# Performance work log

Measured on AMD Instinct MI355X. Metric: run time of the kernel, lower is better.

The kernel has to match this reference:

```python
import jax, jax.numpy as jnp
import numpy as np

EPS = 1e-6   # param.eps
DT = 1e-2    # param.dt
DX = 1.0     # param.dx
DY = 1.0     # param.dy
N_PARAM = 1.0  # param.N


def _lap(c, dx=1.0, dy=1.0):
    # 5-point periodic Laplacian stencil on the last two dims
    return ((jnp.roll(c, 1, -1) + jnp.roll(c, -1, -1) - 2.0 * c) / (dx * dx)
            + (jnp.roll(c, 1, -2) + jnp.roll(c, -1, -2) - 2.0 * c) / (dy * dy))


def _log_with_mask(m, eps=EPS):
    # masked positions get constant eps -> zero gradient there, like torch masked_fill
    return jnp.log(jnp.where(m < eps, eps, m))


def setup_inputs() -> dict:
    key = jax.random.key(0)
    ks = jax.random.split(key, 12)
    B, H, W = 8, 1024, 1024
    inp = {
        "cv": jax.random.uniform(ks[0], (B, H, W), dtype=jnp.float32),
        "ci": jax.random.uniform(ks[1], (B, H, W), dtype=jnp.float32),
        "eta": jax.random.uniform(ks[2], (B, H, W), dtype=jnp.float32),
    }
    names = ["energy_v0", "energy_i0", "kBT0", "kappa_v0", "kappa_i0",
             "kappa_eta0", "diff_v0", "diff_i0", "L0"]
    for i, n in enumerate(names):
        inp[n] = jax.random.uniform(ks[3 + i], (1,), dtype=jnp.float32)
    return inp


def reference(cv, ci, eta, energy_v0, energy_i0, kBT0, kappa_v0, kappa_i0,
              kappa_eta0, diff_v0, diff_i0, L0):
    energy_v = jnp.abs(energy_v0) + 0.001
    energy_i = jnp.abs(energy_i0) + 0.001
    kBT = jnp.abs(kBT0) + 0.001
    kappa_v = jnp.abs(kappa_v0) + 0.001
    kappa_i = jnp.abs(kappa_i0) + 0.001
    kappa_eta = jnp.abs(kappa_eta0) + 0.001
    diff_v = jnp.abs(diff_v0) + 0.001
    diff_i = jnp.abs(diff_i0) + 0.001
    L = jnp.abs(L0) + 0.001

    lap_cv = _lap(cv, DX, DY)
    lap_ci = _lap(ci, DX, DY)
    lap_eta = _lap(eta, DX, DY)

    h = (eta - 1.0) ** 2
    j = eta ** 2
    cs = 1.0 - cv - ci
    log_cv = _log_with_mask(cv)
    log_ci = _log_with_mask(ci)
    log_cs = _log_with_mask(cs)

    fs = energy_v * cv + energy_i * ci + kBT * (cv * log_cv + ci * log_ci + cs * log_cs)
    dfs_dcv = energy_v + kBT * (log_cv - log_cs)
    dfs_dci = energy_i + kBT * (log_ci - log_cs)

    fv = (cv - 1.0) ** 2 + ci ** 2
    dfv_dcv = 2.0 * (cv - 1.0)
    dfv_dci = 2.0 * ci

    dF_dcv = h * dfs_dcv + j * dfv_dcv - kappa_v * lap_cv
    dF_dci = h * dfs_dci + j * dfv_dci - kappa_i * lap_ci
    dF_deta = N_PARAM * (fs * 2.0 * (eta - 1.0) + fv * 2.0 * eta - kappa_eta * lap_eta)

    mv = diff_v * cv / kBT
    mi = diff_i * ci / kBT

    cv_new = jnp.clip(cv + DT * (mv * _lap(dF_dcv)), 0.0, 1.0)
    ci_new = jnp.clip(ci + DT * (mi * _lap(dF_dci)), 0.0, 1.0)
    eta_new = jnp.clip(eta + DT * (-L * dF_deta), 0.0, 1.0)
    return cv_new, ci_new, eta_new
```

## Files before the change

### kernel.cpp

```cpp
#include <hip/hip_runtime.h>

#define WMASK 1023
#define LOG2W 10
#define HW (1024 * 1024)

#define EPS 1e-6f
#define DT 1e-2f

#define TX 64
#define TY 16
#define RX 72
#define RY 20
#define DXT 66
#define DYT 18

__device__ __forceinline__ float scal(const float* __restrict__ p) {
    return fabsf(p[0]) + 0.001f;
}
__device__ __forceinline__ float logm(float m) {
    return __logf(m < EPS ? EPS : m);
}
__device__ __forceinline__ float clip01(float v) {
    return fminf(fmaxf(v, 0.0f), 1.0f);
}

__global__ __launch_bounds__(256) void irr_fused(
    const float* __restrict__ cv,
    const float* __restrict__ ci,
    const float* __restrict__ eta,
    const float* __restrict__ p_ev,
    const float* __restrict__ p_ei,
    const float* __restrict__ p_kbt,
    const float* __restrict__ p_kv,
    const float* __restrict__ p_ki,
    const float* __restrict__ p_ke,
    const float* __restrict__ p_dv,
    const float* __restrict__ p_di,
    const float* __restrict__ p_L,
    float* __restrict__ cv_new,
    float* __restrict__ ci_new,
    float* __restrict__ eta_new)
{
    __shared__ float scv[RY][RX];
    __shared__ float sci[RY][RX];
    __shared__ float seta[RY][RX];
    __shared__ float sdv[DYT][DXT];
    __shared__ float sdi[DYT][DXT];

    const int tid = threadIdx.x;
    const int x0 = blockIdx.x * TX;
    const int y0 = blockIdx.y * TY;
    const int bbase = blockIdx.z * HW;

    const float energy_v = scal(p_ev);
    const float energy_i = scal(p_ei);
    const float kBT      = scal(p_kbt);
    const float kappa_v  = scal(p_kv);
    const float kappa_i  = scal(p_ki);
    const float kappa_e  = scal(p_ke);
    const float diff_v   = scal(p_dv);
    const float diff_i   = scal(p_di);
    const float L        = scal(p_L);
    const float rv = diff_v / kBT;
    const float ri = diff_i / kBT;

    for (int t = tid; t < 3 * 384; t += 256) {
        const int f = t / 384;
        const int r = t - f * 384;
        if (r < 360) {
            const int cx = r % 18;
            const int cy = r / 18;
            const int gx = (x0 - 4 + cx * 4) & WMASK;
            const int gy = (y0 - 2 + cy) & WMASK;
            const float* __restrict__ src = (f == 0) ? cv : (f == 1) ? ci : eta;
            const float4 v = *(const float4*)(src + bbase + (gy << LOG2W) + gx);
            float* dst = (f == 0) ? &scv[cy][cx * 4]
                       : (f == 1) ? &sci[cy][cx * 4]
                                  : &seta[cy][cx * 4];
            *(float4*)dst = v;
        }
    }
    __syncthreads();

    for (int t = tid; t < DXT * DYT; t += 256) {
        const int ex = t % DXT;
        const int ey = t / DXT;
        const int rx = ex + 3;
        const int ry = ey + 1;

        const float c0 = scv[ry][rx];
        const float lap_cv = scv[ry][rx - 1] + scv[ry][rx + 1]
                           + scv[ry - 1][rx] + scv[ry + 1][rx] - 4.0f * c0;
        const float i0 = sci[ry][rx];
        const float lap_ci = sci[ry][rx - 1] + sci[ry][rx + 1]
                           + sci[ry - 1][rx] + sci[ry + 1][rx] - 4.0f * i0;
        const float e0 = seta[ry][rx];
        const float lap_eta = seta[ry][rx - 1] + seta[ry][rx + 1]
                            + seta[ry - 1][rx] + seta[ry + 1][rx] - 4.0f * e0;

        const float h  = (e0 - 1.0f) * (e0 - 1.0f);
        const float jj = e0 * e0;
        const float cs = 1.0f - c0 - i0;
        const float lcv = logm(c0);
        const float lci = logm(i0);
        const float lcs = logm(cs);

        const float fs = energy_v * c0 + energy_i * i0
                       + kBT * (c0 * lcv + i0 * lci + cs * lcs);
        const float dfs_dcv = energy_v + kBT * (lcv - lcs);
        const float dfs_dci = energy_i + kBT * (lci - lcs);

        const float fv = (c0 - 1.0f) * (c0 - 1.0f) + i0 * i0;

        sdv[ey][ex] = h * dfs_dcv + jj * (2.0f * (c0 - 1.0f)) - kappa_v * lap_cv;
        sdi[ey][ex] = h * dfs_dci + jj * (2.0f * i0)          - kappa_i * lap_ci;

        if (ex >= 1 && ex <= TX && ey >= 1 && ey <= TY) {
            const float dF_deta = fs * 2.0f * (e0 - 1.0f) + fv * 2.0f * e0
                                - kappa_e * lap_eta;
            const int gidx = bbase + ((y0 + ey - 1) << LOG2W) + (x0 + ex - 1);
            __builtin_nontemporal_store(clip01(e0 + DT * (-L * dF_deta)),
                                        &eta_new[gidx]);
        }
    }
    __syncthreads();

    for (int t = tid; t < TX * TY; t += 256) {
        const int ox = t & (TX - 1);
        const int oy = t >> 6;
        const int ex = ox + 1;
        const int ey = oy + 1;

        const float v0 = sdv[ey][ex];
        const float lap_v = sdv[ey][ex - 1] + sdv[ey][ex + 1]
                          + sdv[ey - 1][ex] + sdv[ey + 1][ex] - 4.0f * v0;
        const float w0 = sdi[ey][ex];
        const float lap_i = sdi[ey][ex - 1] + sdi[ey][ex + 1]
                          + sdi[ey - 1][ex] + sdi[ey + 1][ex] - 4.0f * w0;

        const float c0 = scv[oy + 2][ox + 4];
        const float i0 = sci[oy + 2][ox + 4];

        const int gidx = bbase + ((y0 + oy) << LOG2W) + (x0 + ox);
        __builtin_nontemporal_store(clip01(c0 + DT * ((rv * c0) * lap_v)), &cv_new[gidx]);
        __builtin_nontemporal_store(clip01(i0 + DT * ((ri * i0) * lap_i)), &ci_new[gidx]);
    }
}

extern "C" void kernel_launch(void* const* d_in, const int* in_sizes, int n_in,
                              void* d_out, int out_size, void* d_ws, size_t ws_size,
                              hipStream_t stream) {
    const float* cv  = (const float*)d_in[0];
    const float* ci  = (const float*)d_in[1];
    const float* eta = (const float*)d_in[2];
    const float* p_ev  = (const float*)d_in[3];
    const float* p_ei  = (const float*)d_in[4];
    const float* p_kbt = (const float*)d_in[5];
    const float* p_kv  = (const float*)d_in[6];
    const float* p_ki  = (const float*)d_in[7];
    const float* p_ke  = (const float*)d_in[8];
    const float* p_dv  = (const float*)d_in[9];
    const float* p_di  = (const float*)d_in[10];
    const float* p_L   = (const float*)d_in[11];

    const int N = in_sizes[0];

    float* out     = (float*)d_out;
    float* cv_new  = out;
    float* ci_new  = out + N;
    float* eta_new = out + 2 * N;

    const dim3 block(256);
    const dim3 grid(1024 / TX, 1024 / TY, N / HW);

    irr_fused<<<grid, block, 0, stream>>>(cv, ci, eta, p_ev, p_ei, p_kbt,
                                          p_kv, p_ki, p_ke, p_dv, p_di, p_L,
                                          cv_new, ci_new, eta_new);
}
```

Before: 208.3 us.

## Vectorize stencil stages to process four columns per thread with float4 LDS access

Reworks the shared-memory layout to 80-column padded rows aligned to float4 and has each thread in the intermediate and final stencil stages compute four adjacent columns. LDS reads and writes and global stores become 128-bit vector operations instead of scalar ones. The intermediate stage computes a 72-wide halo, slightly more redundant work, in exchange for aligned vector access and less index arithmetic. Register pressure rises from unrolled four-wide computation.

```diff
diff --git a/kernel.cpp b/kernel.cpp
--- a/kernel.cpp
+++ b/kernel.cpp
@@ -9,10 +9,11 @@
 
 #define TX 64
 #define TY 16
-#define RX 72
-#define RY 20
-#define DXT 66
-#define DYT 18
+#define RXP 80
+#define RYH 20
+#define DYH 18
+
+typedef float f4 __attribute__((ext_vector_type(4)));
 
 __device__ __forceinline__ float scal(const float* __restrict__ p) {
     return fabsf(p[0]) + 0.001f;
@@ -41,11 +42,11 @@
     float* __restrict__ ci_new,
     float* __restrict__ eta_new)
 {
-    __shared__ float scv[RY][RX];
-    __shared__ float sci[RY][RX];
-    __shared__ float seta[RY][RX];
-    __shared__ float sdv[DYT][DXT];
-    __shared__ float sdi[DYT][DXT];
+    __shared__ float scv[RYH][RXP];
+    __shared__ float sci[RYH][RXP];
+    __shared__ float seta[RYH][RXP];
+    __shared__ float sdv[DYH][RXP];
+    __shared__ float sdi[DYH][RXP];
 
     const int tid = threadIdx.x;
     const int x0 = blockIdx.x * TX;
@@ -58,92 +59,140 @@
     const float kappa_v  = scal(p_kv);
     const float kappa_i  = scal(p_ki);
     const float kappa_e  = scal(p_ke);
-    const float diff_v   = scal(p_dv);
-    const float diff_i   = scal(p_di);
     const float L        = scal(p_L);
-    const float rv = diff_v / kBT;
-    const float ri = diff_i / kBT;
-
-    for (int t = tid; t < 3 * 384; t += 256) {
-        const int f = t / 384;
-        const int r = t - f * 384;
-        if (r < 360) {
-            const int cx = r % 18;
-            const int cy = r / 18;
-            const int gx = (x0 - 4 + cx * 4) & WMASK;
-            const int gy = (y0 - 2 + cy) & WMASK;
-            const float* __restrict__ src = (f == 0) ? cv : (f == 1) ? ci : eta;
-            const float4 v = *(const float4*)(src + bbase + (gy << LOG2W) + gx);
-            float* dst = (f == 0) ? &scv[cy][cx * 4]
-                       : (f == 1) ? &sci[cy][cx * 4]
-                                  : &seta[cy][cx * 4];
-            *(float4*)dst = v;
+    const float rv = scal(p_dv) / kBT;
+    const float ri = scal(p_di) / kBT;
+
+    for (int t = tid; t < 1080; t += 256) {
+        const int f  = t / 360;
+        const int r  = t - f * 360;
+        const int cy = r / 18;
+        const int c  = r - cy * 18 + 1;
+        const int gx = (x0 + 4 * c - 8) & WMASK;
+        const int gy = (y0 - 2 + cy) & WMASK;
+        const float* __restrict__ src = (f == 0) ? cv : (f == 1) ? ci : eta;
+        const f4 v = *(const f4*)(src + bbase + (gy << LOG2W) + gx);
+        float* dst = (f == 0) ? &scv[cy][4 * c]
+                   : (f == 1) ? &sci[cy][4 * c]
+                              : &seta[cy][4 * c];
+        *(f4*)dst = v;
+    }
+    __syncthreads();
+
+    for (int t = tid; t < 324; t += 256) {
+        const int row = t / 18;
+        const int c   = t - row * 18 + 1;
+        const int col = 4 * c;
+        const int ry  = row + 1;
+
+        const f4 cM4 = *(const f4*)&scv[ry][col];
+        const float cL = scv[ry][col - 1];
+        const float cR = scv[ry][col + 4];
+        const f4 cU4 = *(const f4*)&scv[ry - 1][col];
+        const f4 cD4 = *(const f4*)&scv[ry + 1][col];
+
+        const f4 iM4 = *(const f4*)&sci[ry][col];
+        const float iL = sci[ry][col - 1];
+        const float iR = sci[ry][col + 4];
+        const f4 iU4 = *(const f4*)&sci[ry - 1][col];
+        const f4 iD4 = *(const f4*)&sci[ry + 1][col];
+
+        const f4 eM4 = *(const f4*)&seta[ry][col];
+        const float eL = seta[ry][col - 1];
+        const float eR = seta[ry][col + 4];
+        const f4 eU4 = *(const f4*)&seta[ry - 1][col];
+        const f4 eD4 = *(const f4*)&seta[ry + 1][col];
+
+        f4 dv4, di4, et4;
+
+#pragma unroll
+        for (int j = 0; j < 4; ++j) {
+            const float c0 = cM4[j];
+            const float i0 = iM4[j];
+            const float e0 = eM4[j];
+            const float cxl = (j == 0) ? cL : cM4[j - 1];
+            const float cxr = (j == 3) ? cR : cM4[j + 1];
+            const float ixl = (j == 0) ? iL : iM4[j - 1];
+            const float ixr = (j == 3) ? iR : iM4[j + 1];
+            const float exl = (j == 0) ? eL : eM4[j - 1];
+            const float exr = (j == 3) ? eR : eM4[j + 1];
+
+            const float lap_cv  = cxl + cxr + cU4[j] + cD4[j] - 4.0f * c0;
+            const float lap_ci  = ixl + ixr + iU4[j] + iD4[j] - 4.0f * i0;
+            const float lap_eta = exl + exr + eU4[j] + eD4[j] - 4.0f * e0;
+
+            const float h  = (e0 - 1.0f) * (e0 - 1.0f);
+            const float jj = e0 * e0;
+            const float cs = 1.0f - c0 - i0;
+            const float lcv = logm(c0);
+            const float lci = logm(i0);
+            const float lcs = logm(cs);
+
+            const float fs = energy_v * c0 + energy_i * i0
+                           + kBT * (c0 * lcv + i0 * lci + cs * lcs);
+            const float dfs_dcv = energy_v + kBT * (lcv - lcs);
+            const float dfs_dci = energy_i + kBT * (lci - lcs);
+            const float fv = (c0 - 1.0f) * (c0 - 1.0f) + i0 * i0;
+
+            dv4[j] = h * dfs_dcv + jj * (2.0f * (c0 - 1.0f)) - kappa_v * lap_cv;
+            di4[j] = h * dfs_dci + jj * (2.0f * i0)          - kappa_i * lap_ci;
+            const float dF_deta = fs * 2.0f * (e0 - 1.0f) + fv * 2.0f * e0
+                                - kappa_e * lap_eta;
+            et4[j] = clip01(e0 + DT * (-L * dF_deta));
+        }
+
+        *(f4*)&sdv[row][col] = dv4;
+        *(f4*)&sdi[row][col] = di4;
+
+        if (c >= 2 && c <= 17 && row >= 1 && row <= 16) {
+            const int gidx = bbase + ((y0 + row - 1) << LOG2W) + (x0 + col - 8);
+            __builtin_nontemporal_store(et4, (f4*)&eta_new[gidx]);
         }
     }
     __syncthreads();
 
-    for (int t = tid; t < DXT * DYT; t += 256) {
-        const int ex = t % DXT;
-        const int ey = t / DXT;
-        const int rx = ex + 3;
-        const int ry = ey + 1;
-
-        const float c0 = scv[ry][rx];
-        const float lap_cv = scv[ry][rx - 1] + scv[ry][rx + 1]
-                           + scv[ry - 1][rx] + scv[ry + 1][rx] - 4.0f * c0;
-        const float i0 = sci[ry][rx];
-        const float lap_ci = sci[ry][rx - 1] + sci[ry][rx + 1]
-                           + sci[ry - 1][rx] + sci[ry + 1][rx] - 4.0f * i0;
-        const float e0 = seta[ry][rx];
-        const float lap_eta = seta[ry][rx - 1] + seta[ry][rx + 1]
-                            + seta[ry - 1][rx] + seta[ry + 1][rx] - 4.0f * e0;
-
-        const float h  = (e0 - 1.0f) * (e0 - 1.0f);
-        const float jj = e0 * e0;
-        const float cs = 1.0f - c0 - i0;
-        const float lcv = logm(c0);
-        const float lci = logm(i0);
-        const float lcs = logm(cs);
-
-        const float fs = energy_v * c0 + energy_i * i0
-                       + kBT * (c0 * lcv + i0 * lci + cs * lcs);
-        const float dfs_dcv = energy_v + kBT * (lcv - lcs);
-        const float dfs_dci = energy_i + kBT * (lci - lcs);
-
-        const float fv = (c0 - 1.0f) * (c0 - 1.0f) + i0 * i0;
-
-        sdv[ey][ex] = h * dfs_dcv + jj * (2.0f * (c0 - 1.0f)) - kappa_v * lap_cv;
-        sdi[ey][ex] = h * dfs_dci + jj * (2.0f * i0)          - kappa_i * lap_ci;
-
-        if (ex >= 1 && ex <= TX && ey >= 1 && ey <= TY) {
-            const float dF_deta = fs * 2.0f * (e0 - 1.0f) + fv * 2.0f * e0
-                                - kappa_e * lap_eta;
-            const int gidx = bbase + ((y0 + ey - 1) << LOG2W) + (x0 + ex - 1);
-            __builtin_nontemporal_store(clip01(e0 + DT * (-L * dF_deta)),
-                                        &eta_new[gidx]);
+    {
+        const int oy  = tid >> 4;
+        const int cg  = tid & 15;
+        const int col = 8 + 4 * cg;
+        const int ey  = oy + 1;
+
+        const f4 vM4 = *(const f4*)&sdv[ey][col];
+        const float vL = sdv[ey][col - 1];
+        const float vR = sdv[ey][col + 4];
+        const f4 vU4 = *(const f4*)&sdv[ey - 1][col];
+        const f4 vD4 = *(const f4*)&sdv[ey + 1][col];
+
+        const f4 wM4 = *(const f4*)&sdi[ey][col];
+        const float wL = sdi[ey][col - 1];
+        const float wR = sdi[ey][col + 4];
+        const f4 wU4 = *(const f4*)&sdi[ey - 1][col];
+        const f4 wD4 = *(const f4*)&sdi[ey + 1][col];
+
+        const f4 c4 = *(const f4*)&scv[oy + 2][col];
+        const f4 i4 = *(const f4*)&sci[oy + 2][col];
+
+        f4 cvo, cio;
+
+#pragma unroll
+        for (int j = 0; j < 4; ++j) {
+            const float v0 = vM4[j];
+            const float w0 = wM4[j];
+            const float vxl = (j == 0) ? vL : vM4[j - 1];
+            const float vxr = (j == 3) ? vR : vM4[j + 1];
+            const float wxl = (j == 0) ? wL : wM4[j - 1];
+            const float wxr = (j == 3) ? wR : wM4[j + 1];
+
+            const float lap_v = vxl + vxr + vU4[j] + vD4[j] - 4.0f * v0;
+            const float lap_w = wxl + wxr + wU4[j] + wD4[j] - 4.0f * w0;
+
+            cvo[j] = clip01(c4[j] + DT * ((rv * c4[j]) * lap_v));
+            cio[j] = clip01(i4[j] + DT * ((ri * i4[j]) * lap_w));
         }
-    }
-    __syncthreads();
-
-    for (int t = tid; t < TX * TY; t += 256) {
-        const int ox = t & (TX - 1);
-        const int oy = t >> 6;
-        const int ex = ox + 1;
-        const int ey = oy + 1;
-
-        const float v0 = sdv[ey][ex];
-        const float lap_v = sdv[ey][ex - 1] + sdv[ey][ex + 1]
-                          + sdv[ey - 1][ex] + sdv[ey + 1][ex] - 4.0f * v0;
-        const float w0 = sdi[ey][ex];
-        const float lap_i = sdi[ey][ex - 1] + sdi[ey][ex + 1]
-                          + sdi[ey - 1][ex] + sdi[ey + 1][ex] - 4.0f * w0;
-
-        const float c0 = scv[oy + 2][ox + 4];
-        const float i0 = sci[oy + 2][ox + 4];
-
-        const int gidx = bbase + ((y0 + oy) << LOG2W) + (x0 + ox);
-        __builtin_nontemporal_store(clip01(c0 + DT * ((rv * c0) * lap_v)), &cv_new[gidx]);
-        __builtin_nontemporal_store(clip01(i0 + DT * ((ri * i0) * lap_i)), &ci_new[gidx]);
+
+        const int gidx = bbase + ((y0 + oy) << LOG2W) + (x0 + 4 * cg);
+        __builtin_nontemporal_store(cvo, (f4*)&cv_new[gidx]);
+        __builtin_nontemporal_store(cio, (f4*)&ci_new[gidx]);
     }
 }
 
```

After: 213.6 us. +2.5%, slower.
